# Optimization experiments

Measured on AMD Instinct MI355X. Metric: run time of the kernel, lower is better.

## Reference

```python
import jax, jax.numpy as jnp
import numpy as np

# static config matching init_kwargs / input_specs
D = 768      # dim
H = 12       # num_heads
HD = D // H  # head_dim = 64
C = 38       # in_chans (AlternatingAttention default)
B = 4
T = 256
N = C * T    # 9728
SCALE = HD ** -0.5
EPS = 1e-5   # LayerNorm eps
HID = 4 * D  # mlp hidden


def setup_inputs() -> dict:
    key = jax.random.key(0)
    ks = jax.random.split(key, 6)
    w = lambda k, sh: (jax.random.normal(k, sh, jnp.float32) * 0.02)
    return {
        "x": jax.random.normal(ks[0], (B, N, D), jnp.float32),
        "norm1_w": jnp.ones((D,), jnp.float32),
        "norm1_b": jnp.zeros((D,), jnp.float32),
        "qkv_w": w(ks[1], (3 * D, D)),            # nn.Linear(dim, 3*dim, bias=False)
        "proj_w": w(ks[2], (D, D)),
        "proj_b": jnp.zeros((D,), jnp.float32),
        "norm2_w": jnp.ones((D,), jnp.float32),
        "norm2_b": jnp.zeros((D,), jnp.float32),
        "fc1_w": w(ks[3], (HID, D)),
        "fc1_b": jnp.zeros((HID,), jnp.float32),
        "fc2_w": w(ks[4], (D, HID)),
        "fc2_b": jnp.zeros((D,), jnp.float32),
    }


def _ln(x, w, b):
    m = x.mean(-1, keepdims=True)
    v = ((x - m) ** 2).mean(-1, keepdims=True)
    return (x - m) * jax.lax.rsqrt(v + EPS) * w + b


def _attn(x, qkv_w, proj_w, proj_b):
    # x: (Bc, Nn, D) -- manual (non-fused) SDPA as in the torch module
    Bc, Nn, _ = x.shape
    qkv = (x @ qkv_w.T).reshape(Bc, Nn, 3, H, HD)
    q, k, v = jnp.moveaxis(qkv, 2, 0)             # each (Bc, Nn, H, HD)
    q = jnp.swapaxes(q, 1, 2) * SCALE             # (Bc, H, Nn, HD)
    k = jnp.swapaxes(k, 1, 2)
    v = jnp.swapaxes(v, 1, 2)
    attn = jax.nn.softmax(q @ jnp.swapaxes(k, -2, -1), axis=-1)  # (Bc,H,Nn,Nn)
    o = attn @ v                                  # (Bc, H, Nn, HD)
    o = jnp.swapaxes(o, 1, 2).reshape(Bc, Nn, D)
    return o @ proj_w.T + proj_b


def reference(x, norm1_w, norm1_b, qkv_w, proj_w, proj_b,
              norm2_w, norm2_b, fc1_w, fc1_b, fc2_w, fc2_b):
    # Attention branch: block_idx=1 -> time-axis attention
    h = _ln(x, norm1_w, norm1_b)
    h = h.reshape(B, C, T, D).reshape(B * C, T, D)   # 'B (C T) D -> (B C) T D'
    h = _attn(h, qkv_w, proj_w, proj_b)
    h = h.reshape(B, C, T, D).reshape(B, N, D)       # '(B C) T D -> B (C T) D'
    x = x + h                                        # ls1 = Identity, drop_path = Identity
    # MLP branch
    h2 = _ln(x, norm2_w, norm2_b)
    h2 = jax.nn.gelu(h2 @ fc1_w.T + fc1_b, approximate=False)
    h2 = h2 @ fc2_w.T + fc2_b
    return x + h2
```

## Files before the change

### kernel.cpp

```cpp
#include <hip/hip_runtime.h>
#include <stdint.h>

#define DD 768
#define HH 12
#define HDIM 64
#define TT 256
#define BCN 152
#define MROWS 38912
#define HID 3072

typedef __attribute__((ext_vector_type(8))) short bf16x8;
typedef __attribute__((ext_vector_type(4))) float f32x4;

__device__ __forceinline__ float b2f(unsigned short u) {
  union { unsigned int i; float f; } c; c.i = ((unsigned int)u) << 16; return c.f;
}
__device__ __forceinline__ unsigned short f2b(float f) {
  union { float f; unsigned int i; } c; c.f = f;
  unsigned int x = c.i;
  return (unsigned short)((x + 0x7fffu + ((x >> 16) & 1u)) >> 16);
}

__device__ __forceinline__ void gload16(const unsigned short* g, unsigned short* l) {
  __builtin_amdgcn_global_load_lds(
      (const __attribute__((address_space(1))) void*)g,
      (__attribute__((address_space(3))) void*)l, 16, 0, 0);
}

__global__ __launch_bounds__(256) void k_cvt(const float* __restrict__ in,
                                             unsigned short* __restrict__ out, int n4) {
  int i = blockIdx.x * 256 + threadIdx.x;
  if (i >= n4) return;
  float4 a = ((const float4*)in)[i];
  ushort4 u;
  u.x = f2b(a.x); u.y = f2b(a.y); u.z = f2b(a.z); u.w = f2b(a.w);
  ((ushort4*)out)[i] = u;
}

__global__ __launch_bounds__(256) void k_ln(const float* __restrict__ x,
                                            const float* __restrict__ w,
                                            const float* __restrict__ b,
                                            unsigned short* __restrict__ out) {
  int lane = threadIdx.x & 63;
  int wv = threadIdx.x >> 6;
  size_t row = (size_t)blockIdx.x * 4 + wv;
  const float4* xr = (const float4*)(x + row * DD);
  float4 v0 = xr[lane], v1 = xr[lane + 64], v2 = xr[lane + 128];
  float s = v0.x + v0.y + v0.z + v0.w + v1.x + v1.y + v1.z + v1.w + v2.x + v2.y + v2.z + v2.w;
  float q = v0.x*v0.x + v0.y*v0.y + v0.z*v0.z + v0.w*v0.w
          + v1.x*v1.x + v1.y*v1.y + v1.z*v1.z + v1.w*v1.w
          + v2.x*v2.x + v2.y*v2.y + v2.z*v2.z + v2.w*v2.w;
#pragma unroll
  for (int m = 1; m < 64; m <<= 1) { s += __shfl_xor(s, m, 64); q += __shfl_xor(q, m, 64); }
  float mean = s * (1.0f / 768.0f);
  float var = q * (1.0f / 768.0f) - mean * mean;
  float rstd = rsqrtf(var + 1e-5f);
  ushort4* orow = (ushort4*)(out + row * DD);
#pragma unroll
  for (int i = 0; i < 3; i++) {
    int idx = lane + i * 64;
    float4 v = (i == 0) ? v0 : (i == 1) ? v1 : v2;
    float4 ww = ((const float4*)w)[idx];
    float4 bb = ((const float4*)b)[idx];
    ushort4 u;
    u.x = f2b((v.x - mean) * rstd * ww.x + bb.x);
    u.y = f2b((v.y - mean) * rstd * ww.y + bb.y);
    u.z = f2b((v.z - mean) * rstd * ww.z + bb.z);
    u.w = f2b((v.w - mean) * rstd * ww.w + bb.w);
    orow[idx] = u;
  }
}

template <int MODE>
__global__ __launch_bounds__(256, 4) void k_gemm6(const unsigned short* __restrict__ A,
                                                  const unsigned short* __restrict__ W,
                                                  const float* __restrict__ bias,
                                                  const float* resid,
                                                  void* outv, int N, int K) {
  __shared__ __align__(16) unsigned short As[128 * 64];
  __shared__ __align__(16) unsigned short Bs[128 * 64];
  const int tid = threadIdx.x;
  const int lane = tid & 63, wv = tid >> 6;
  const int wr = wv >> 1, wc = wv & 1;
  const int cl = lane & 15, hi = lane >> 4;

  const int nbx = gridDim.x;
  const int nwg = nbx * gridDim.y;
  const int flat = blockIdx.y * nbx + blockIdx.x;
  const int swz = (flat & 7) * (nwg >> 3) + (flat >> 3);
  const size_t bm = (size_t)(swz / nbx) * 128;
  const size_t bn = (size_t)(swz % nbx) * 128;
  const unsigned short* Ab = A + bm * K;
  const unsigned short* Wb = W + bn * K;

  f32x4 acc[4][4];
#pragma unroll
  for (int m = 0; m < 4; m++)
#pragma unroll
    for (int n = 0; n < 4; n++) acc[m][n] = (f32x4){0.f, 0.f, 0.f, 0.f};

  const int nk = K >> 6;
  for (int kt = 0; kt < nk; ++kt) {
    __syncthreads();
#pragma unroll
    for (int i = 0; i < 4; i++) {
      int g = i * 256 + tid;
      int row = g >> 3;
      int cg = (g & 7) ^ (row & 7);
      gload16(Ab + (size_t)row * K + (size_t)kt * 64 + cg * 8, &As[g * 8]);
      gload16(Wb + (size_t)row * K + (size_t)kt * 64 + cg * 8, &Bs[g * 8]);
    }
    __syncthreads();
#pragma unroll
    for (int ks = 0; ks < 2; ++ks) {
      bf16x8 af[4], bfr[4];
#pragma unroll
      for (int m = 0; m < 4; m++) {
        int row = wr * 64 + m * 16 + cl;
        af[m] = *(const bf16x8*)&As[row * 64 + (((ks * 4 + hi) ^ (row & 7)) * 8)];
      }
#pragma unroll
      for (int n = 0; n < 4; n++) {
        int row = wc * 64 + n * 16 + cl;
        bfr[n] = *(const bf16x8*)&Bs[row * 64 + (((ks * 4 + hi) ^ (row & 7)) * 8)];
      }
#pragma unroll
      for (int m = 0; m < 4; m++)
#pragma unroll
        for (int n = 0; n < 4; n++)
          acc[m][n] = __builtin_amdgcn_mfma_f32_16x16x32_bf16(af[m], bfr[n], acc[m][n], 0, 0, 0);
    }
  }

#pragma unroll
  for (int m = 0; m < 4; m++) {
#pragma unroll
    for (int n = 0; n < 4; n++) {
      size_t col = bn + wc * 64 + n * 16 + cl;
#pragma unroll
      for (int r = 0; r < 4; r++) {
        size_t row = bm + wr * 64 + m * 16 + hi * 4 + r;
        float v = acc[m][n][r];
        if (MODE == 0) {
          ((unsigned short*)outv)[row * N + col] = f2b(v);
        } else if (MODE == 1) {
          v += bias[col] + resid[row * N + col];
          ((float*)outv)[row * N + col] = v;
        } else {
          v += bias[col];
          float g = 0.5f * v * (1.0f + erff(v * 0.70710678118654752f));
          ((unsigned short*)outv)[row * N + col] = f2b(g);
        }
      }
    }
  }
}

__global__ __launch_bounds__(512) void k_attn(const unsigned short* __restrict__ qkv,
                                              unsigned short* __restrict__ o) {
  __shared__ __align__(16) unsigned short Kc[2][64 * 64];
  __shared__ __align__(16) unsigned short Vt[64 * 64];
  __shared__ __align__(16) unsigned short Pl[8][16 * 64];
  const int h = blockIdx.x, bc = blockIdx.y;
  const int tid = threadIdx.x;
  const int lane = tid & 63, wv = tid >> 6;
  const int cl = lane & 15, hi = lane >> 4;

  bf16x8 qf[2][2];
#pragma unroll
  for (int m = 0; m < 2; m++)
#pragma unroll
    for (int ks = 0; ks < 2; ks++) {
      size_t row = (size_t)bc * 256 + wv * 32 + m * 16 + cl;
      bf16x8 raw = *(const bf16x8*)(qkv + row * 2304 + h * 64 + ks * 32 + hi * 8);
      bf16x8 sc;
#pragma unroll
      for (int jx = 0; jx < 8; jx++) sc[jx] = (short)f2b(0.125f * b2f((unsigned short)raw[jx]));
      qf[m][ks] = sc;
    }

  f32x4 oacc[2][4];
#pragma unroll
  for (int m = 0; m < 2; m++)
#pragma unroll
    for (int n = 0; n < 4; n++) oacc[m][n] = (f32x4){0.f, 0.f, 0.f, 0.f};
  float mrun[2][4], lrun[2][4];
#pragma unroll
  for (int m = 0; m < 2; m++)
#pragma unroll
    for (int r = 0; r < 4; r++) { mrun[m][r] = -1e30f; lrun[m][r] = 0.f; }

  auto stageK = [&](int j, int buf) {
    int tok = tid >> 3, c8 = tid & 7;
    size_t gtok = (size_t)bc * 256 + j * 64 + tok;
    gload16(qkv + gtok * 2304 + 768 + h * 64 + ((c8 ^ (tok & 7)) * 8), &Kc[buf][tid * 8]);
  };
  uint4 vreg[2];
  auto loadV = [&](int j, int slot) {
    int tok = tid >> 3, c8 = tid & 7;
    size_t gtok = (size_t)bc * 256 + j * 64 + tok;
    vreg[slot] = *(const uint4*)(qkv + gtok * 2304 + 1536 + h * 64 + c8 * 8);
  };
  auto writeV = [&](int slot) {
    int tok = tid >> 3, c8 = tid & 7;
    union { uint4 u4; unsigned short us[8]; } cv; cv.u4 = vreg[slot];
#pragma unroll
    for (int jj = 0; jj < 8; jj++) {
      int d = c8 * 8 + jj;
      int g = ((tok >> 3) ^ (d & 7) ^ ((d >> 3) & 7)) & 7;
      Vt[d * 64 + g * 8 + (tok & 7)] = cv.us[jj];
    }
  };

  stageK(0, 0);
  loadV(0, 0);

  for (int j = 0; j < 4; j++) {
    __syncthreads();

    f32x4 s[2][4];
#pragma unroll
    for (int m = 0; m < 2; m++)
#pragma unroll
      for (int n = 0; n < 4; n++) s[m][n] = (f32x4){0.f, 0.f, 0.f, 0.f};
#pragma unroll
    for (int ks = 0; ks < 2; ++ks) {
      bf16x8 kf[4];
#pragma unroll
      for (int n = 0; n < 4; n++) {
        int row = n * 16 + cl;
        kf[n] = *(const bf16x8*)&Kc[j & 1][row * 64 + (((ks * 4 + hi) ^ (row & 7)) * 8)];
      }
#pragma unroll
      for (int m = 0; m < 2; m++)
#pragma unroll
        for (int n = 0; n < 4; n++)
          s[m][n] = __builtin_amdgcn_mfma_f32_16x16x32_bf16(qf[m][ks], kf[n], s[m][n], 0, 0, 0);
    }

    stageK((j + 1) & 3, (j + 1) & 1);
    loadV((j + 1) & 3, (j + 1) & 1);

#pragma unroll
    for (int m = 0; m < 2; m++) {
#pragma unroll
      for (int r = 0; r < 4; r++) {
        float pm = fmaxf(fmaxf(s[m][0][r], s[m][1][r]), fmaxf(s[m][2][r], s[m][3][r]));
#pragma unroll
        for (int xm = 1; xm < 16; xm <<= 1) pm = fmaxf(pm, __shfl_xor(pm, xm, 64));
        float nm = fmaxf(mrun[m][r], pm);
        float fac = __expf(mrun[m][r] - nm);
        mrun[m][r] = nm;
        float ps = 0.f;
#pragma unroll
        for (int n = 0; n < 4; n++) {
          float e = __expf(s[m][n][r] - nm);
          s[m][n][r] = e;
          ps += e;
        }
#pragma unroll
        for (int xm = 1; xm < 16; xm <<= 1) ps += __shfl_xor(ps, xm, 64);
        lrun[m][r] = lrun[m][r] * fac + ps;
#pragma unroll
        for (int n2 = 0; n2 < 4; n2++) oacc[m][n2][r] *= fac;
      }
    }

    writeV(j & 1);
    __syncthreads();

    bf16x8 pv[2][4];
#pragma unroll
    for (int ks = 0; ks < 2; ks++)
#pragma unroll
      for (int n = 0; n < 4; n++) {
        int d = n * 16 + cl;
        pv[ks][n] = *(const bf16x8*)&Vt[d * 64 + ((((ks * 4 + hi) ^ (d & 7) ^ ((d >> 3) & 7)) & 7) * 8)];
      }
#pragma unroll
    for (int m = 0; m < 2; m++) {
#pragma unroll
      for (int n = 0; n < 4; n++)
#pragma unroll
        for (int r = 0; r < 4; r++) {
          int q = hi * 4 + r;
          int g = ((n * 2 + (cl >> 3)) ^ (q & 7) ^ (q >> 3)) & 7;
          Pl[wv][q * 64 + g * 8 + (cl & 7)] = f2b(s[m][n][r]);
        }
      asm volatile("s_waitcnt lgkmcnt(0)" ::: "memory");
      __builtin_amdgcn_sched_barrier(0);
      bf16x8 pa0 = *(const bf16x8*)&Pl[wv][cl * 64 + (((hi ^ (cl & 7) ^ (cl >> 3)) & 7) * 8)];
      bf16x8 pa1 = *(const bf16x8*)&Pl[wv][cl * 64 + ((((4 + hi) ^ (cl & 7) ^ (cl >> 3)) & 7) * 8)];
#pragma unroll
      for (int n = 0; n < 4; n++)
        oacc[m][n] = __builtin_amdgcn_mfma_f32_16x16x32_bf16(pa0, pv[0][n], oacc[m][n], 0, 0, 0);
#pragma unroll
      for (int n = 0; n < 4; n++)
        oacc[m][n] = __builtin_amdgcn_mfma_f32_16x16x32_bf16(pa1, pv[1][n], oacc[m][n], 0, 0, 0);
    }
  }

#pragma unroll
  for (int m = 0; m < 2; m++)
#pragma unroll
    for (int r = 0; r < 4; r++) {
      float inv = 1.0f / lrun[m][r];
      size_t row = (size_t)bc * 256 + wv * 32 + m * 16 + hi * 4 + r;
#pragma unroll
      for (int n = 0; n < 4; n++)
        o[row * DD + h * 64 + n * 16 + cl] = f2b(oacc[m][n][r] * inv);
    }
}

extern "C" void kernel_launch(void* const* d_in, const int* in_sizes, int n_in,
                              void* d_out, int out_size, void* d_ws, size_t ws_size,
                              hipStream_t stream) {
  const float* x     = (const float*)d_in[0];
  const float* n1w   = (const float*)d_in[1];
  const float* n1b   = (const float*)d_in[2];
  const float* qkvw  = (const float*)d_in[3];
  const float* projw = (const float*)d_in[4];
  const float* projb = (const float*)d_in[5];
  const float* n2w   = (const float*)d_in[6];
  const float* n2b   = (const float*)d_in[7];
  const float* fc1w  = (const float*)d_in[8];
  const float* fc1b  = (const float*)d_in[9];
  const float* fc2w  = (const float*)d_in[10];
  const float* fc2b  = (const float*)d_in[11];
  float* out = (float*)d_out;

  const size_t NEED = 312999936ull;
  if (ws_size < NEED) return;
  char* ws = (char*)d_ws;
  unsigned short* h   = (unsigned short*)(ws);
  unsigned short* qkv = (unsigned short*)(ws + 59768832ull);
  unsigned short* ob  = (unsigned short*)(ws + 239075328ull);
  unsigned short* act = (unsigned short*)(ws + 59768832ull);
  unsigned short* wq  = (unsigned short*)(ws + 298844160ull);
  unsigned short* wp  = wq + 2304 * 768;
  unsigned short* w1  = wp + 768 * 768;
  unsigned short* w2  = w1 + 3072 * 768;

  k_cvt<<<1728, 256, 0, stream>>>(qkvw, wq, 2304 * 768 / 4);
  k_cvt<<<576, 256, 0, stream>>>(projw, wp, 768 * 768 / 4);
  k_cvt<<<2304, 256, 0, stream>>>(fc1w, w1, 3072 * 768 / 4);
  k_cvt<<<2304, 256, 0, stream>>>(fc2w, w2, 768 * 3072 / 4);

  k_ln<<<MROWS / 4, 256, 0, stream>>>(x, n1w, n1b, h);
  k_gemm6<0><<<dim3(2304 / 128, MROWS / 128), 256, 0, stream>>>(h, wq, nullptr, nullptr, qkv, 2304, 768);
  k_attn<<<dim3(HH, BCN), 512, 0, stream>>>(qkv, ob);
  k_gemm6<1><<<dim3(768 / 128, MROWS / 128), 256, 0, stream>>>(ob, wp, projb, x, out, 768, 768);
  k_ln<<<MROWS / 4, 256, 0, stream>>>(out, n2w, n2b, h);
  k_gemm6<2><<<dim3(3072 / 128, MROWS / 128), 256, 0, stream>>>(h, w1, fc1b, nullptr, act, 3072, 768);
  k_gemm6<1><<<dim3(768 / 128, MROWS / 128), 256, 0, stream>>>(act, w2, fc2b, out, out, 768, 3072);
}
```

Measured before the change: 1.012 ms.

## Replace GEMM with 256x256-tile, 8-wave, double-buffered ping-pong pipelined kernel

Replaces the 128x128 single-buffered GEMM with a 256x256 tile kernel using 512 threads, double-buffered LDS, and an interleaved schedule. The schedule issues global-to-LDS loads for later k-steps between quarter-tile MFMA batches, using explicit waitcnt, barriers and setprio. This is meant to hide memory latency and raise arithmetic intensity per loaded byte. The trade-offs are one block per CU with 128KB of LDS and fewer workgroups, which leaves 456 blocks for the N=768 GEMMs on 256 CUs and risks a tail effect.

```diff
diff --git a/kernel.cpp b/kernel.cpp
--- a/kernel.cpp
+++ b/kernel.cpp
@@ -71,89 +71,182 @@
   }
 }
 
+
+template <int MH>
+__device__ __forceinline__ void read_a(const unsigned short* Al, bf16x8 (&af)[4][2],
+                                       int wr, int cl, int hi) {
+#pragma unroll
+  for (int mi = 0; mi < 4; mi++)
+#pragma unroll
+    for (int ks = 0; ks < 2; ks++) {
+      int row = MH * 128 + wr * 64 + mi * 16 + cl;
+      af[mi][ks] = *(const bf16x8*)&Al[row * 64 + (((ks * 4 + hi) ^ (row & 7)) * 8)];
+    }
+}
+
+template <int G>
+__device__ __forceinline__ void read_b(const unsigned short* Bl, bf16x8 (&bfr)[2][2][2],
+                                       int wc, int cl, int hi) {
+#pragma unroll
+  for (int ni = 0; ni < 2; ni++)
+#pragma unroll
+    for (int ks = 0; ks < 2; ks++) {
+      int row = G * 128 + wc * 32 + ni * 16 + cl;
+      bfr[G][ni][ks] = *(const bf16x8*)&Bl[row * 64 + (((ks * 4 + hi) ^ (row & 7)) * 8)];
+    }
+}
+
+template <int MH, int G>
+__device__ __forceinline__ void mfma_q(f32x4 (&acc)[2][4][2][2], const bf16x8 (&af)[4][2],
+                                       const bf16x8 (&bfr)[2][2][2]) {
+  __builtin_amdgcn_s_setprio(1);
+#pragma unroll
+  for (int mi = 0; mi < 4; mi++)
+#pragma unroll
+    for (int ni = 0; ni < 2; ni++)
+#pragma unroll
+      for (int ks = 0; ks < 2; ks++)
+        acc[MH][mi][G][ni] = __builtin_amdgcn_mfma_f32_16x16x32_bf16(
+            af[mi][ks], bfr[G][ni][ks], acc[MH][mi][G][ni], 0, 0, 0);
+  __builtin_amdgcn_s_setprio(0);
+}
+
+#define VM6   asm volatile("s_waitcnt vmcnt(6)" ::: "memory")
+#define VM0   asm volatile("s_waitcnt vmcnt(0)" ::: "memory")
+#define LGKM0 do { asm volatile("s_waitcnt lgkmcnt(0)" ::: "memory"); \
+                   __builtin_amdgcn_sched_barrier(0); } while (0)
+#define BAR   __builtin_amdgcn_s_barrier()
+
 template <int MODE>
-__global__ __launch_bounds__(256, 4) void k_gemm6(const unsigned short* __restrict__ A,
+__global__ __launch_bounds__(512, 1) void k_gemm8(const unsigned short* __restrict__ A,
                                                   const unsigned short* __restrict__ W,
                                                   const float* __restrict__ bias,
                                                   const float* resid,
                                                   void* outv, int N, int K) {
-  __shared__ __align__(16) unsigned short As[128 * 64];
-  __shared__ __align__(16) unsigned short Bs[128 * 64];
+  __shared__ __align__(16) unsigned short As[2][256 * 64];
+  __shared__ __align__(16) unsigned short Bs[2][256 * 64];
   const int tid = threadIdx.x;
   const int lane = tid & 63, wv = tid >> 6;
-  const int wr = wv >> 1, wc = wv & 1;
+  const int wr = wv >> 2, wc = wv & 3;
   const int cl = lane & 15, hi = lane >> 4;
 
   const int nbx = gridDim.x;
   const int nwg = nbx * gridDim.y;
   const int flat = blockIdx.y * nbx + blockIdx.x;
   const int swz = (flat & 7) * (nwg >> 3) + (flat >> 3);
-  const size_t bm = (size_t)(swz / nbx) * 128;
-  const size_t bn = (size_t)(swz % nbx) * 128;
+  const size_t bm = (size_t)(swz / nbx) * 256;
+  const size_t bn = (size_t)(swz % nbx) * 256;
   const unsigned short* Ab = A + bm * K;
   const unsigned short* Wb = W + bn * K;
 
-  f32x4 acc[4][4];
-#pragma unroll
-  for (int m = 0; m < 4; m++)
-#pragma unroll
-    for (int n = 0; n < 4; n++) acc[m][n] = (f32x4){0.f, 0.f, 0.f, 0.f};
-
-  const int nk = K >> 6;
-  for (int kt = 0; kt < nk; ++kt) {
-    __syncthreads();
-#pragma unroll
-    for (int i = 0; i < 4; i++) {
-      int g = i * 256 + tid;
-      int row = g >> 3;
-      int cg = (g & 7) ^ (row & 7);
-      gload16(Ab + (size_t)row * K + (size_t)kt * 64 + cg * 8, &As[g * 8]);
-      gload16(Wb + (size_t)row * K + (size_t)kt * 64 + cg * 8, &Bs[g * 8]);
-    }
-    __syncthreads();
-#pragma unroll
-    for (int ks = 0; ks < 2; ++ks) {
-      bf16x8 af[4], bfr[4];
-#pragma unroll
-      for (int m = 0; m < 4; m++) {
-        int row = wr * 64 + m * 16 + cl;
-        af[m] = *(const bf16x8*)&As[row * 64 + (((ks * 4 + hi) ^ (row & 7)) * 8)];
-      }
-#pragma unroll
-      for (int n = 0; n < 4; n++) {
-        int row = wc * 64 + n * 16 + cl;
-        bfr[n] = *(const bf16x8*)&Bs[row * 64 + (((ks * 4 + hi) ^ (row & 7)) * 8)];
-      }
-#pragma unroll
-      for (int m = 0; m < 4; m++)
-#pragma unroll
-        for (int n = 0; n < 4; n++)
-          acc[m][n] = __builtin_amdgcn_mfma_f32_16x16x32_bf16(af[m], bfr[n], acc[m][n], 0, 0, 0);
-    }
+  auto stA = [&](int kt, int bb, int h) {
+#pragma unroll
+    for (int j = 0; j < 2; j++) {
+      int idx = j * 512 + tid;
+      int row = h * 128 + (idx >> 3);
+      int cg = (idx & 7) ^ (row & 7);
+      gload16(Ab + (size_t)row * K + (size_t)kt * 64 + cg * 8,
+              &As[bb][row * 64 + (idx & 7) * 8]);
+    }
+  };
+  auto stB = [&](int kt, int bb, int h) {
+#pragma unroll
+    for (int j = 0; j < 2; j++) {
+      int idx = j * 512 + tid;
+      int row = h * 128 + (idx >> 3);
+      int cg = (idx & 7) ^ (row & 7);
+      gload16(Wb + (size_t)row * K + (size_t)kt * 64 + cg * 8,
+              &Bs[bb][row * 64 + (idx & 7) * 8]);
+    }
+  };
+
+  f32x4 acc[2][4][2][2];
+#pragma unroll
+  for (int a0 = 0; a0 < 2; a0++)
+#pragma unroll
+    for (int a1 = 0; a1 < 4; a1++)
+#pragma unroll
+      for (int a2 = 0; a2 < 2; a2++)
+#pragma unroll
+        for (int a3 = 0; a3 < 2; a3++) acc[a0][a1][a2][a3] = (f32x4){0.f, 0.f, 0.f, 0.f};
+
+  bf16x8 af[4][2], bfr[2][2][2];
+  const int nt = K >> 6;
+
+  stA(0, 0, 0); stB(0, 0, 0); stB(0, 0, 1); stA(0, 0, 1);
+  stA(1, 1, 0); stB(1, 1, 0); stA(1, 1, 1);
+  VM6;
+  BAR;
+
+  for (int t = 0; t < nt; t += 2) {
+    const bool more = (t + 2) < nt;
+    read_a<0>(As[0], af, wr, cl, hi);
+    read_b<0>(Bs[0], bfr, wc, cl, hi);
+    stB(t + 1, 1, 1);
+    BAR; LGKM0;
+    mfma_q<0, 0>(acc, af, bfr);
+    BAR;
+    read_b<1>(Bs[0], bfr, wc, cl, hi);
+    if (more) stA(t + 2, 0, 0);
+    BAR; LGKM0;
+    mfma_q<0, 1>(acc, af, bfr);
+    BAR;
+    read_a<1>(As[0], af, wr, cl, hi);
+    if (more) stB(t + 2, 0, 0);
+    BAR; LGKM0;
+    mfma_q<1, 0>(acc, af, bfr);
+    BAR;
+    if (more) { stA(t + 2, 0, 1); VM6; } else { VM0; }
+    BAR;
+    mfma_q<1, 1>(acc, af, bfr);
+    BAR;
+    read_a<0>(As[1], af, wr, cl, hi);
+    read_b<0>(Bs[1], bfr, wc, cl, hi);
+    if (more) stB(t + 2, 0, 1);
+    BAR; LGKM0;
+    mfma_q<0, 0>(acc, af, bfr);
+    BAR;
+    read_b<1>(Bs[1], bfr, wc, cl, hi);
+    if (more) stA(t + 3, 1, 0);
+    BAR; LGKM0;
+    mfma_q<0, 1>(acc, af, bfr);
+    BAR;
+    read_a<1>(As[1], af, wr, cl, hi);
+    if (more) stB(t + 3, 1, 0);
+    BAR; LGKM0;
+    mfma_q<1, 0>(acc, af, bfr);
+    BAR;
+    if (more) { stA(t + 3, 1, 1); VM6; }
+    BAR;
+    mfma_q<1, 1>(acc, af, bfr);
+    BAR;
   }
 
 #pragma unroll
-  for (int m = 0; m < 4; m++) {
-#pragma unroll
-    for (int n = 0; n < 4; n++) {
-      size_t col = bn + wc * 64 + n * 16 + cl;
-#pragma unroll
-      for (int r = 0; r < 4; r++) {
-        size_t row = bm + wr * 64 + m * 16 + hi * 4 + r;
-        float v = acc[m][n][r];
-        if (MODE == 0) {
-          ((unsigned short*)outv)[row * N + col] = f2b(v);
-        } else if (MODE == 1) {
-          v += bias[col] + resid[row * N + col];
-          ((float*)outv)[row * N + col] = v;
-        } else {
-          v += bias[col];
-          float g = 0.5f * v * (1.0f + erff(v * 0.70710678118654752f));
-          ((unsigned short*)outv)[row * N + col] = f2b(g);
+  for (int mh = 0; mh < 2; mh++)
+#pragma unroll
+    for (int mi = 0; mi < 4; mi++)
+#pragma unroll
+      for (int g = 0; g < 2; g++)
+#pragma unroll
+        for (int ni = 0; ni < 2; ni++) {
+          size_t col = bn + g * 128 + wc * 32 + ni * 16 + cl;
+#pragma unroll
+          for (int rr = 0; rr < 4; rr++) {
+            size_t row = bm + mh * 128 + wr * 64 + mi * 16 + hi * 4 + rr;
+            float v = acc[mh][mi][g][ni][rr];
+            if (MODE == 0) {
+              ((unsigned short*)outv)[row * N + col] = f2b(v);
+            } else if (MODE == 1) {
+              v += bias[col] + resid[row * N + col];
+              ((float*)outv)[row * N + col] = v;
+            } else {
+              v += bias[col];
+              float gg = 0.5f * v * (1.0f + erff(v * 0.70710678118654752f));
+              ((unsigned short*)outv)[row * N + col] = f2b(gg);
+            }
+          }
         }
-      }
-    }
-  }
 }
 
 __global__ __launch_bounds__(512) void k_attn(const unsigned short* __restrict__ qkv,
@@ -347,10 +440,10 @@
   k_cvt<<<2304, 256, 0, stream>>>(fc2w, w2, 768 * 3072 / 4);
 
   k_ln<<<MROWS / 4, 256, 0, stream>>>(x, n1w, n1b, h);
-  k_gemm6<0><<<dim3(2304 / 128, MROWS / 128), 256, 0, stream>>>(h, wq, nullptr, nullptr, qkv, 2304, 768);
+  k_gemm8<0><<<dim3(2304 / 256, MROWS / 256), 512, 0, stream>>>(h, wq, nullptr, nullptr, qkv, 2304, 768);
   k_attn<<<dim3(HH, BCN), 512, 0, stream>>>(qkv, ob);
-  k_gemm6<1><<<dim3(768 / 128, MROWS / 128), 256, 0, stream>>>(ob, wp, projb, x, out, 768, 768);
+  k_gemm8<1><<<dim3(768 / 256, MROWS / 256), 512, 0, stream>>>(ob, wp, projb, x, out, 768, 768);
   k_ln<<<MROWS / 4, 256, 0, stream>>>(out, n2w, n2b, h);
-  k_gemm6<2><<<dim3(3072 / 128, MROWS / 128), 256, 0, stream>>>(h, w1, fc1b, nullptr, act, 3072, 768);
-  k_gemm6<1><<<dim3(768 / 128, MROWS / 128), 256, 0, stream>>>(act, w2, fc2b, out, out, 768, 3072);
-}
+  k_gemm8<2><<<dim3(3072 / 256, MROWS / 256), 512, 0, stream>>>(h, w1, fc1b, nullptr, act, 3072, 768);
+  k_gemm8<1><<<dim3(768 / 256, MROWS / 256), 512, 0, stream>>>(act, w2, fc2b, out, out, 768, 3072);
+}
```

Measured after the change: 1.132 ms. +11.8%, slower.

## Split attention query rows across grid z with smaller 4-wave blocks

Applied to the files above, without the earlier changes.

The attention kernel now launches four blocks per (head, sequence), each handling 64 query rows with 4 waves of 16 rows, instead of one 8-wave block covering all 256 queries. This cuts per-wave register state and raises block count and occupancy. The cost is that each block restages the full K and V tiles, quadrupling K/V reads, and the V prefetch is reordered after the LDS transpose write.

```diff
diff --git a/kernel.cpp b/kernel.cpp
--- a/kernel.cpp
+++ b/kernel.cpp
@@ -156,73 +156,78 @@
   }
 }
 
-__global__ __launch_bounds__(512) void k_attn(const unsigned short* __restrict__ qkv,
-                                              unsigned short* __restrict__ o) {
+__global__ __launch_bounds__(256, 4) void k_attn(const unsigned short* __restrict__ qkv,
+                                                 unsigned short* __restrict__ o) {
   __shared__ __align__(16) unsigned short Kc[2][64 * 64];
   __shared__ __align__(16) unsigned short Vt[64 * 64];
-  __shared__ __align__(16) unsigned short Pl[8][16 * 64];
-  const int h = blockIdx.x, bc = blockIdx.y;
+  __shared__ __align__(16) unsigned short Pl[4][16 * 64];
+  const int h = blockIdx.x, bc = blockIdx.y, qz = blockIdx.z;
   const int tid = threadIdx.x;
   const int lane = tid & 63, wv = tid >> 6;
   const int cl = lane & 15, hi = lane >> 4;
-
-  bf16x8 qf[2][2];
-#pragma unroll
-  for (int m = 0; m < 2; m++)
-#pragma unroll
-    for (int ks = 0; ks < 2; ks++) {
-      size_t row = (size_t)bc * 256 + wv * 32 + m * 16 + cl;
-      bf16x8 raw = *(const bf16x8*)(qkv + row * 2304 + h * 64 + ks * 32 + hi * 8);
-      bf16x8 sc;
-#pragma unroll
-      for (int jx = 0; jx < 8; jx++) sc[jx] = (short)f2b(0.125f * b2f((unsigned short)raw[jx]));
-      qf[m][ks] = sc;
-    }
-
-  f32x4 oacc[2][4];
-#pragma unroll
-  for (int m = 0; m < 2; m++)
-#pragma unroll
-    for (int n = 0; n < 4; n++) oacc[m][n] = (f32x4){0.f, 0.f, 0.f, 0.f};
-  float mrun[2][4], lrun[2][4];
-#pragma unroll
-  for (int m = 0; m < 2; m++)
-#pragma unroll
-    for (int r = 0; r < 4; r++) { mrun[m][r] = -1e30f; lrun[m][r] = 0.f; }
+  const int qb = qz * 64 + wv * 16;
+
+  bf16x8 qf[2];
+#pragma unroll
+  for (int ks = 0; ks < 2; ks++) {
+    size_t row = (size_t)bc * 256 + qb + cl;
+    bf16x8 raw = *(const bf16x8*)(qkv + row * 2304 + h * 64 + ks * 32 + hi * 8);
+    bf16x8 sc;
+#pragma unroll
+    for (int jx = 0; jx < 8; jx++) sc[jx] = (short)f2b(0.125f * b2f((unsigned short)raw[jx]));
+    qf[ks] = sc;
+  }
+
+  f32x4 oacc[4];
+#pragma unroll
+  for (int n = 0; n < 4; n++) oacc[n] = (f32x4){0.f, 0.f, 0.f, 0.f};
+  float mrun[4], lrun[4];
+#pragma unroll
+  for (int r = 0; r < 4; r++) { mrun[r] = -1e30f; lrun[r] = 0.f; }
 
   auto stageK = [&](int j, int buf) {
-    int tok = tid >> 3, c8 = tid & 7;
-    size_t gtok = (size_t)bc * 256 + j * 64 + tok;
-    gload16(qkv + gtok * 2304 + 768 + h * 64 + ((c8 ^ (tok & 7)) * 8), &Kc[buf][tid * 8]);
+#pragma unroll
+    for (int i = 0; i < 2; i++) {
+      int idx = i * 256 + tid;
+      int tok = idx >> 3, c8 = idx & 7;
+      size_t gtok = (size_t)bc * 256 + j * 64 + tok;
+      gload16(qkv + gtok * 2304 + 768 + h * 64 + ((c8 ^ (tok & 7)) * 8), &Kc[buf][idx * 8]);
+    }
   };
   uint4 vreg[2];
-  auto loadV = [&](int j, int slot) {
-    int tok = tid >> 3, c8 = tid & 7;
-    size_t gtok = (size_t)bc * 256 + j * 64 + tok;
-    vreg[slot] = *(const uint4*)(qkv + gtok * 2304 + 1536 + h * 64 + c8 * 8);
+  auto loadV = [&](int j) {
+#pragma unroll
+    for (int i = 0; i < 2; i++) {
+      int idx = i * 256 + tid;
+      int tok = idx >> 3, c8 = idx & 7;
+      size_t gtok = (size_t)bc * 256 + j * 64 + tok;
+      vreg[i] = *(const uint4*)(qkv + gtok * 2304 + 1536 + h * 64 + c8 * 8);
+    }
   };
-  auto writeV = [&](int slot) {
-    int tok = tid >> 3, c8 = tid & 7;
-    union { uint4 u4; unsigned short us[8]; } cv; cv.u4 = vreg[slot];
-#pragma unroll
-    for (int jj = 0; jj < 8; jj++) {
-      int d = c8 * 8 + jj;
-      int g = ((tok >> 3) ^ (d & 7) ^ ((d >> 3) & 7)) & 7;
-      Vt[d * 64 + g * 8 + (tok & 7)] = cv.us[jj];
+  auto writeV = [&]() {
+#pragma unroll
+    for (int i = 0; i < 2; i++) {
+      int idx = i * 256 + tid;
+      int tok = idx >> 3, c8 = idx & 7;
+      union { uint4 u4; unsigned short us[8]; } cv; cv.u4 = vreg[i];
+#pragma unroll
+      for (int jj = 0; jj < 8; jj++) {
+        int d = c8 * 8 + jj;
+        int g = ((tok >> 3) ^ (d & 7) ^ ((d >> 3) & 7)) & 7;
+        Vt[d * 64 + g * 8 + (tok & 7)] = cv.us[jj];
+      }
     }
   };
 
   stageK(0, 0);
-  loadV(0, 0);
+  loadV(0);
 
   for (int j = 0; j < 4; j++) {
     __syncthreads();
 
-    f32x4 s[2][4];
-#pragma unroll
-    for (int m = 0; m < 2; m++)
-#pragma unroll
-      for (int n = 0; n < 4; n++) s[m][n] = (f32x4){0.f, 0.f, 0.f, 0.f};
+    f32x4 s[4];
+#pragma unroll
+    for (int n = 0; n < 4; n++) s[n] = (f32x4){0.f, 0.f, 0.f, 0.f};
 #pragma unroll
     for (int ks = 0; ks < 2; ++ks) {
       bf16x8 kf[4];
@@ -232,41 +237,36 @@
         kf[n] = *(const bf16x8*)&Kc[j & 1][row * 64 + (((ks * 4 + hi) ^ (row & 7)) * 8)];
       }
 #pragma unroll
-      for (int m = 0; m < 2; m++)
-#pragma unroll
-        for (int n = 0; n < 4; n++)
-          s[m][n] = __builtin_amdgcn_mfma_f32_16x16x32_bf16(qf[m][ks], kf[n], s[m][n], 0, 0, 0);
+      for (int n = 0; n < 4; n++)
+        s[n] = __builtin_amdgcn_mfma_f32_16x16x32_bf16(qf[ks], kf[n], s[n], 0, 0, 0);
     }
 
     stageK((j + 1) & 3, (j + 1) & 1);
-    loadV((j + 1) & 3, (j + 1) & 1);
-
-#pragma unroll
-    for (int m = 0; m < 2; m++) {
-#pragma unroll
-      for (int r = 0; r < 4; r++) {
-        float pm = fmaxf(fmaxf(s[m][0][r], s[m][1][r]), fmaxf(s[m][2][r], s[m][3][r]));
-#pragma unroll
-        for (int xm = 1; xm < 16; xm <<= 1) pm = fmaxf(pm, __shfl_xor(pm, xm, 64));
-        float nm = fmaxf(mrun[m][r], pm);
-        float fac = __expf(mrun[m][r] - nm);
-        mrun[m][r] = nm;
-        float ps = 0.f;
-#pragma unroll
-        for (int n = 0; n < 4; n++) {
-          float e = __expf(s[m][n][r] - nm);
-          s[m][n][r] = e;
-          ps += e;
-        }
-#pragma unroll
-        for (int xm = 1; xm < 16; xm <<= 1) ps += __shfl_xor(ps, xm, 64);
-        lrun[m][r] = lrun[m][r] * fac + ps;
-#pragma unroll
-        for (int n2 = 0; n2 < 4; n2++) oacc[m][n2][r] *= fac;
-      }
-    }
-
-    writeV(j & 1);
+
+#pragma unroll
+    for (int r = 0; r < 4; r++) {
+      float pm = fmaxf(fmaxf(s[0][r], s[1][r]), fmaxf(s[2][r], s[3][r]));
+#pragma unroll
+      for (int xm = 1; xm < 16; xm <<= 1) pm = fmaxf(pm, __shfl_xor(pm, xm, 64));
+      float nm = fmaxf(mrun[r], pm);
+      float fac = __expf(mrun[r] - nm);
+      mrun[r] = nm;
+      float ps = 0.f;
+#pragma unroll
+      for (int n = 0; n < 4; n++) {
+        float e = __expf(s[n][r] - nm);
+        s[n][r] = e;
+        ps += e;
+      }
+#pragma unroll
+      for (int xm = 1; xm < 16; xm <<= 1) ps += __shfl_xor(ps, xm, 64);
+      lrun[r] = lrun[r] * fac + ps;
+#pragma unroll
+      for (int n2 = 0; n2 < 4; n2++) oacc[n2][r] *= fac;
+    }
+
+    writeV();
+    loadV((j + 1) & 3);
     __syncthreads();
 
     bf16x8 pv[2][4];
@@ -278,38 +278,33 @@
         pv[ks][n] = *(const bf16x8*)&Vt[d * 64 + ((((ks * 4 + hi) ^ (d & 7) ^ ((d >> 3) & 7)) & 7) * 8)];
       }
 #pragma unroll
-    for (int m = 0; m < 2; m++) {
-#pragma unroll
-      for (int n = 0; n < 4; n++)
-#pragma unroll
-        for (int r = 0; r < 4; r++) {
-          int q = hi * 4 + r;
-          int g = ((n * 2 + (cl >> 3)) ^ (q & 7) ^ (q >> 3)) & 7;
-          Pl[wv][q * 64 + g * 8 + (cl & 7)] = f2b(s[m][n][r]);
-        }
-      asm volatile("s_waitcnt lgkmcnt(0)" ::: "memory");
-      __builtin_amdgcn_sched_barrier(0);
-      bf16x8 pa0 = *(const bf16x8*)&Pl[wv][cl * 64 + (((hi ^ (cl & 7) ^ (cl >> 3)) & 7) * 8)];
-      bf16x8 pa1 = *(const bf16x8*)&Pl[wv][cl * 64 + ((((4 + hi) ^ (cl & 7) ^ (cl >> 3)) & 7) * 8)];
-#pragma unroll
-      for (int n = 0; n < 4; n++)
-        oacc[m][n] = __builtin_amdgcn_mfma_f32_16x16x32_bf16(pa0, pv[0][n], oacc[m][n], 0, 0, 0);
-#pragma unroll
-      for (int n = 0; n < 4; n++)
-        oacc[m][n] = __builtin_amdgcn_mfma_f32_16x16x32_bf16(pa1, pv[1][n], oacc[m][n], 0, 0, 0);
-    }
-  }
-
-#pragma unroll
-  for (int m = 0; m < 2; m++)
-#pragma unroll
-    for (int r = 0; r < 4; r++) {
-      float inv = 1.0f / lrun[m][r];
-      size_t row = (size_t)bc * 256 + wv * 32 + m * 16 + hi * 4 + r;
-#pragma unroll
-      for (int n = 0; n < 4; n++)
-        o[row * DD + h * 64 + n * 16 + cl] = f2b(oacc[m][n][r] * inv);
-    }
+    for (int n = 0; n < 4; n++)
+#pragma unroll
+      for (int r = 0; r < 4; r++) {
+        int q = hi * 4 + r;
+        int g = ((n * 2 + (cl >> 3)) ^ (q & 7) ^ (q >> 3)) & 7;
+        Pl[wv][q * 64 + g * 8 + (cl & 7)] = f2b(s[n][r]);
+      }
+    asm volatile("s_waitcnt lgkmcnt(0)" ::: "memory");
+    __builtin_amdgcn_sched_barrier(0);
+    bf16x8 pa0 = *(const bf16x8*)&Pl[wv][cl * 64 + (((hi ^ (cl & 7) ^ (cl >> 3)) & 7) * 8)];
+    bf16x8 pa1 = *(const bf16x8*)&Pl[wv][cl * 64 + ((((4 + hi) ^ (cl & 7) ^ (cl >> 3)) & 7) * 8)];
+#pragma unroll
+    for (int n = 0; n < 4; n++)
+      oacc[n] = __builtin_amdgcn_mfma_f32_16x16x32_bf16(pa0, pv[0][n], oacc[n], 0, 0, 0);
+#pragma unroll
+    for (int n = 0; n < 4; n++)
+      oacc[n] = __builtin_amdgcn_mfma_f32_16x16x32_bf16(pa1, pv[1][n], oacc[n], 0, 0, 0);
+  }
+
+#pragma unroll
+  for (int r = 0; r < 4; r++) {
+    float inv = 1.0f / lrun[r];
+    size_t row = (size_t)bc * 256 + qb + hi * 4 + r;
+#pragma unroll
+    for (int n = 0; n < 4; n++)
+      o[row * DD + h * 64 + n * 16 + cl] = f2b(oacc[n][r] * inv);
+  }
 }
 
 extern "C" void kernel_launch(void* const* d_in, const int* in_sizes, int n_in,
@@ -348,7 +343,7 @@
 
   k_ln<<<MROWS / 4, 256, 0, stream>>>(x, n1w, n1b, h);
   k_gemm6<0><<<dim3(2304 / 128, MROWS / 128), 256, 0, stream>>>(h, wq, nullptr, nullptr, qkv, 2304, 768);
-  k_attn<<<dim3(HH, BCN), 512, 0, stream>>>(qkv, ob);
+  k_attn<<<dim3(HH, BCN, 4), 256, 0, stream>>>(qkv, ob);
   k_gemm6<1><<<dim3(768 / 128, MROWS / 128), 256, 0, stream>>>(ob, wp, projb, x, out, 768, 768);
   k_ln<<<MROWS / 4, 256, 0, stream>>>(out, n2w, n2b, h);
   k_gemm6<2><<<dim3(3072 / 128, MROWS / 128), 256, 0, stream>>>(h, w1, fc1b, nullptr, act, 3072, 768);
```

Measured after the change: 1.001 ms. About the same (-1.1%).
